# Kernel optimization log

Hardware: AMD Instinct MI355X
Metric: run time of the kernel (lower is better)

## Reference

```python
import jax, jax.numpy as jnp
import numpy as np
from functools import partial

B, H, W = 2, 480, 480
C, HALF = 32, 16
L, WN, PAD = 4, 20, 20

def gelu(x):
    return jax.nn.gelu(x, approximate=False)

def setup_inputs() -> dict:
    key = jax.random.key(0)
    ks = jax.random.split(key, 24)
    scale = 1.0 / (C * C)
    d = {}
    d["input_data"] = jax.random.normal(ks[0], (B, H, W, 1), jnp.float32)
    d["src_data"] = jax.random.normal(ks[1], (B, H, W, 3), jnp.float32)
    # input lifting MLP: sizes [5, 16, 32]
    d["in_w1"] = jax.random.normal(ks[2], (5, HALF), jnp.float32) * 0.1
    d["in_b1"] = jnp.zeros((HALF,), jnp.float32)
    d["in_w2"] = jax.random.normal(ks[3], (HALF, C), jnp.float32) * 0.1
    d["in_b2"] = jnp.zeros((C,), jnp.float32)
    # eps lifting MLP: sizes [3, 16, 32]
    d["eps_w1"] = jax.random.normal(ks[4], (3, HALF), jnp.float32) * 0.1
    d["eps_b1"] = jnp.zeros((HALF,), jnp.float32)
    d["eps_w2"] = jax.random.normal(ks[5], (HALF, C), jnp.float32) * 0.1
    d["eps_b2"] = jnp.zeros((C,), jnp.float32)
    # Fourier layer params, stacked over L layers
    d["fw1"] = jax.random.uniform(ks[6], (L, C, C, WN, WN, 2), jnp.float32) * scale
    d["fw2"] = jax.random.uniform(ks[7], (L, C, C, WN, WN, 2), jnp.float32) * scale
    d["conv_w"] = jax.random.normal(ks[8], (L, C, C), jnp.float32) * 0.05
    d["conv_b"] = jnp.zeros((L, C), jnp.float32)
    # projection MLP: sizes [32, 16, 2]
    d["proj_w1"] = jax.random.normal(ks[9], (C, HALF), jnp.float32) * 0.1
    d["proj_b1"] = jnp.zeros((HALF,), jnp.float32)
    d["proj_w2"] = jax.random.normal(ks[10], (HALF, 2), jnp.float32) * 0.1
    d["proj_b2"] = jnp.zeros((2,), jnp.float32)
    # mask conv 3x3, 1->1 channel
    d["mask_w"] = jax.random.normal(ks[11], (1, 1, 3, 3), jnp.float32) * 0.1
    d["mask_b"] = jnp.zeros((1,), jnp.float32)
    return d

def _grid(b, h, w):
    gx = jnp.broadcast_to(jnp.linspace(0.0, 1.0, h, dtype=jnp.float32)[None, :, None, None], (b, h, w, 1))
    gy = jnp.broadcast_to(jnp.linspace(0.0, 1.0, w, dtype=jnp.float32)[None, None, :, None], (b, h, w, 1))
    return jnp.concatenate([gx, gy], axis=-1)

def _mlp(x, w1, b1, w2, b2):
    # FCLayer(gelu) then FCLayer(linear)
    return gelu(x @ w1 + b1) @ w2 + b2

def _fourier_conv(x, x_eps, w1, w2):
    # x, x_eps: [B, C, Hp, Wp]
    hp, wp = x.shape[-2], x.shape[-1]
    xf = jnp.fft.rfft2(x * x_eps)                       # [B,C,Hp,Wp//2+1] complex
    xr = jnp.stack([xf.real, xf.imag], axis=-1)         # [B,C,Hp,Wp//2+1,2]
    lo = jnp.einsum('bixyz,ioxyz->boxyz', xr[:, :, :WN, :WN, :], w1)
    hi = jnp.einsum('bixyz,ioxyz->boxyz', xr[:, :, -WN:, :WN, :], w2)
    out = jnp.zeros((x.shape[0], w1.shape[1], hp, wp // 2 + 1, 2), jnp.float32)
    out = out.at[:, :, :WN, :WN, :].set(lo)
    out = out.at[:, :, -WN:, :WN, :].set(hi)
    return jnp.fft.irfft2(out[..., 0] + 1j * out[..., 1], s=(hp, wp))

def _forward(input_data, src_data, in_w1, in_b1, in_w2, in_b2,
             eps_w1, eps_b1, eps_w2, eps_b2, fw1, fw2, conv_w, conv_b,
             proj_w1, proj_b1, proj_w2, proj_b2, mask_w, mask_b):
    b, h, w = input_data.shape[0], input_data.shape[1], input_data.shape[2]
    grid = _grid(b, h, w)
    x_in = jnp.concatenate([src_data, grid], axis=-1)       # [B,H,W,5]
    x_eps = jnp.concatenate([input_data, grid], axis=-1)    # [B,H,W,3]
    field = src_data[..., 1:]                               # [B,H,W,2]

    a = _mlp(x_in, in_w1, in_b1, in_w2, in_b2)              # [B,H,W,C]
    a = jnp.transpose(a, (0, 3, 1, 2))                      # [B,C,H,W]
    a = jnp.pad(a, ((0, 0), (0, 0), (0, PAD), (0, PAD)))    # [B,C,H+P,W+P]
    e = _mlp(x_eps, eps_w1, eps_b1, eps_w2, eps_b2)
    e = jnp.transpose(e, (0, 3, 1, 2))
    e = jnp.pad(e, ((0, 0), (0, 0), (0, PAD), (0, PAD)))

    for l in range(L):
        x1 = _fourier_conv(a, e, fw1[l], fw2[l])
        x2 = jnp.einsum('bihw,oi->bohw', a, conv_w[l]) + conv_b[l][None, :, None, None]
        a = x1 + x2
        if l < L - 1:
            a = gelu(a)

    pred = a[..., :-PAD, :-PAD]                             # [B,C,H,W]
    pred = jnp.transpose(pred, (0, 2, 3, 1))                # [B,H,W,C]
    pred = _mlp(pred, proj_w1, proj_b1, proj_w2, proj_b2)   # [B,H,W,2]

    xm = jnp.transpose(input_data, (0, 3, 1, 2))            # [B,1,H,W]
    mask = jax.lax.conv_general_dilated(xm, mask_w, (1, 1), 'SAME',
                                        dimension_numbers=('NCHW', 'OIHW', 'NCHW'))
    mask = mask + mask_b[None, :, None, None]
    mask = jnp.transpose(mask, (0, 2, 3, 1))                # [B,H,W,1] -> broadcasts over 2
    return field * mask + pred

def reference(input_data, src_data, in_w1, in_b1, in_w2, in_b2,
              eps_w1, eps_b1, eps_w2, eps_b2, fw1, fw2, conv_w, conv_b,
              proj_w1, proj_b1, proj_w2, proj_b2, mask_w, mask_b):
    return _forward(input_data, src_data, in_w1, in_b1, in_w2, in_b2,
                    eps_w1, eps_b1, eps_w2, eps_b2, fw1, fw2, conv_w, conv_b,
                    proj_w1, proj_b1, proj_w2, proj_b2, mask_w, mask_b)
```

## Files before the change

### kernel.cpp

```cpp
#include <hip/hip_runtime.h>
#include <hip/hip_bf16.h>

#define BD 2
#define HD 480
#define WD 480
#define CD 32
#define HALFD 16
#define WND 20
#define NP 500
#define PLANE (HD*WD)
#define TWO_PI_OVER_NP 0.012566370614359172954f

typedef __attribute__((ext_vector_type(8))) short bf16x8;
typedef __attribute__((ext_vector_type(4))) float f32x4;

__device__ __forceinline__ float gelu_f(float x) {
    return 0.5f * x * (1.0f + erff(x * 0.70710678118654752f));
}
__device__ __forceinline__ float bfbits2f(short s) {
    unsigned u = ((unsigned)(unsigned short)s) << 16;
    return __uint_as_float(u);
}
__device__ __forceinline__ short bf16s(float v) {
    __hip_bfloat16 b = __float2bfloat16(v);
    return *reinterpret_cast<short*>(&b);
}
__device__ __forceinline__ unsigned pk2(float a, float b) {
    return (unsigned)(unsigned short)bf16s(a) | ((unsigned)(unsigned short)bf16s(b) << 16);
}

__global__ void __launch_bounds__(256) k_ae(
    const float* src, const float* inp,
    const float* iw1, const float* ib1,
    const float* iw2, const float* ib2,
    const float* ew1, const float* eb1,
    const float* ew2, const float* eb2,
    __hip_bfloat16* A, __hip_bfloat16* E)
{
    __shared__ float s_iw1[80], s_ib1[16];
    __shared__ float s_ew1[48], s_eb1[16];
    __shared__ __align__(16) __hip_bfloat16 s_hidA[256 * 24];
    __shared__ __align__(16) __hip_bfloat16 s_hidE[256 * 24];
    __shared__ __align__(16) __hip_bfloat16 s_out[32 * 264];

    int tid = threadIdx.x;
    int lane = tid & 63, wv = tid >> 6;

    if (tid < 80) s_iw1[tid] = iw1[tid];
    if (tid >= 96 && tid < 112) s_ib1[tid - 96] = ib1[tid - 96];
    if (tid >= 128 && tid < 176) s_ew1[tid - 128] = ew1[tid - 128];
    if (tid >= 192 && tid < 208) s_eb1[tid - 192] = eb1[tid - 192];

    int c0 = lane & 15, kg = lane >> 4;
    bf16x8 bIn[2], bEps[2];
    float biasIn[2], biasEps[2];
    #pragma unroll
    for (int nt = 0; nt < 2; nt++) {
        int c = nt * 16 + c0;
        #pragma unroll
        for (int j = 0; j < 8; j++) {
            int k = kg * 8 + j;
            bIn[nt][j]  = (k < 16) ? bf16s(iw2[k * 32 + c]) : (short)0;
            bEps[nt][j] = (k < 16) ? bf16s(ew2[k * 32 + c]) : (short)0;
        }
        biasIn[nt]  = ib2[c];
        biasEps[nt] = eb2[c];
    }
    __syncthreads();

    int gid = blockIdx.x * 256 + tid;
    int b = gid / PLANE;
    int r = gid % PLANE;
    int h = r / WD, w = r % WD;
    float gx = (float)h * (1.0f / 479.0f);
    float gy = (float)w * (1.0f / 479.0f);
    float s0 = src[(size_t)gid * 3 + 0];
    float s1 = src[(size_t)gid * 3 + 1];
    float s2 = src[(size_t)gid * 3 + 2];
    float xi = inp[gid];

    {
        unsigned pk[8];
        #pragma unroll
        for (int j = 0; j < 16; j += 2) {
            float v0 = s_ib1[j]     + s0 * s_iw1[j]     + s1 * s_iw1[16 + j]
                     + s2 * s_iw1[32 + j]     + gx * s_iw1[48 + j]     + gy * s_iw1[64 + j];
            float v1 = s_ib1[j + 1] + s0 * s_iw1[j + 1] + s1 * s_iw1[16 + j + 1]
                     + s2 * s_iw1[32 + j + 1] + gx * s_iw1[48 + j + 1] + gy * s_iw1[64 + j + 1];
            pk[j >> 1] = pk2(gelu_f(v0), gelu_f(v1));
        }
        uint4* d = reinterpret_cast<uint4*>(&s_hidA[tid * 24]);
        d[0] = make_uint4(pk[0], pk[1], pk[2], pk[3]);
        d[1] = make_uint4(pk[4], pk[5], pk[6], pk[7]);
        #pragma unroll
        for (int j = 0; j < 16; j += 2) {
            float v0 = s_eb1[j]     + xi * s_ew1[j]     + gx * s_ew1[16 + j]     + gy * s_ew1[32 + j];
            float v1 = s_eb1[j + 1] + xi * s_ew1[j + 1] + gx * s_ew1[16 + j + 1] + gy * s_ew1[32 + j + 1];
            pk[j >> 1] = pk2(gelu_f(v0), gelu_f(v1));
        }
        uint4* d2 = reinterpret_cast<uint4*>(&s_hidE[tid * 24]);
        d2[0] = make_uint4(pk[0], pk[1], pk[2], pk[3]);
        d2[1] = make_uint4(pk[4], pk[5], pk[6], pk[7]);
    }
    __syncthreads();

    int r0 = (blockIdx.x % 900) * 256;

    #pragma unroll
    for (int pass = 0; pass < 2; pass++) {
        const __hip_bfloat16* hid = pass ? s_hidE : s_hidA;
        #pragma unroll
        for (int t = 0; t < 4; t++) {
            int tile = wv * 4 + t;
            bf16x8 av = {0, 0, 0, 0, 0, 0, 0, 0};
            if (kg < 2)
                av = *reinterpret_cast<const bf16x8*>(&hid[(tile * 16 + c0) * 24 + kg * 8]);
            #pragma unroll
            for (int nt = 0; nt < 2; nt++) {
                f32x4 acc = {0.f, 0.f, 0.f, 0.f};
                bf16x8 bv = pass ? bEps[nt] : bIn[nt];
                acc = __builtin_amdgcn_mfma_f32_16x16x32_bf16(av, bv, acc, 0, 0, 0);
                float bias = pass ? biasEps[nt] : biasIn[nt];
                int ch = nt * 16 + c0;
                int px = tile * 16 + kg * 4;
                unsigned w0 = pk2(acc[0] + bias, acc[1] + bias);
                unsigned w1 = pk2(acc[2] + bias, acc[3] + bias);
                *reinterpret_cast<uint2*>(&s_out[ch * 264 + px]) = make_uint2(w0, w1);
            }
        }
        __syncthreads();
        __hip_bfloat16* dst = (pass ? E : A) + (size_t)b * CD * PLANE + r0;
        #pragma unroll
        for (int i = 0; i < 4; i++) {
            int idx = tid + i * 256;
            int ch = idx >> 5, chunk = idx & 31;
            uint4 v = *reinterpret_cast<const uint4*>(&s_out[ch * 264 + chunk * 8]);
            *reinterpret_cast<uint4*>(&dst[(size_t)ch * PLANE + chunk * 8]) = v;
        }
        __syncthreads();
    }
}

__global__ void k_tables(__hip_bfloat16* T) {
    int e = blockIdx.x * 256 + threadIdx.x;
    if (e >= 435 * 512) return;
    int tile = e >> 9, r = e & 511;
    int lane = r >> 3, j = r & 7;
    float v = 0.0f;
    if (tile < 45) {
        int kt = tile / 3, nt = tile % 3;
        int k = kt * 32 + ((lane >> 4) << 3) + j;
        int n = nt * 16 + (lane & 15);
        if (n < 40) {
            int ky = n >> 1;
            int idx = (k * ky) % NP;
            float ang = (float)idx * TWO_PI_OVER_NP;
            v = (n & 1) ? -sinf(ang) : cosf(ang);
        }
    } else if (tile < 105) {
        int t2 = tile - 45;
        int nt = t2 >> 1, kt = t2 & 1;
        int kk = kt * 32 + ((lane >> 4) << 3) + j;
        int w = nt * 16 + (lane & 15);
        if (kk < 40) {
            int ky = kk >> 1;
            int idx = (ky * w) % NP;
            float ang = (float)idx * TWO_PI_OVER_NP;
            v = (kk & 1) ? -sinf(ang) : cosf(ang);
        }
    } else if (tile < 255) {
        int t2 = tile - 105;
        int kt = t2 / 5, nt = t2 % 5;
        int k = kt * 32 + ((lane >> 4) << 3) + j;
        int n = nt * 16 + (lane & 15);
        int hh = k >> 1, ri = k & 1;
        int kxi = n >> 1, part = n & 1;
        int kx = (kxi < 20) ? kxi : kxi + 460;
        int idx = (kx * hh) % NP;
        float ang = (float)idx * TWO_PI_OVER_NP;
        float c = cosf(ang), s = sinf(ang);
        v = (part == 0) ? (ri == 0 ? c : s) : (ri == 0 ? -s : c);
    } else {
        int t2 = tile - 255;
        int nt = t2 / 3, kt = t2 % 3;
        int k = kt * 32 + ((lane >> 4) << 3) + j;
        int n = nt * 16 + (lane & 15);
        if (k < 80) {
            int kxi = k >> 1, ri = k & 1;
            int hh = n >> 1, part = n & 1;
            int kx = (kxi < 20) ? kxi : kxi + 460;
            int idx = (kx * hh) % NP;
            float ang = (float)idx * TWO_PI_OVER_NP;
            float c = cosf(ang), s = sinf(ang);
            v = (part == 0) ? (ri == 0 ? c : -s) : (ri == 0 ? s : c);
        }
    }
    T[e] = __float2bfloat16(v);
}

__global__ void __launch_bounds__(256) k_F1m(
    const __hip_bfloat16* A, const __hip_bfloat16* E,
    const __hip_bfloat16* Twig, __hip_bfloat16* Y1)
{
    int wv = threadIdx.x >> 6, lane = threadIdx.x & 63;
    int task = blockIdx.x * 4 + wv;
    int bh = task / 6, rem = task % 6;
    int mt = rem & 1, nt = rem >> 1;
    int b = bh / HD, h = bh % HD;
    int c = mt * 16 + (lane & 15);
    int koff = (lane >> 4) << 3;
    size_t base = ((size_t)(b * 32 + c)) * PLANE + (size_t)h * WD + koff;
    const __hip_bfloat16* arow = A + base;
    const __hip_bfloat16* erow = E + base;
    f32x4 acc = {0.f, 0.f, 0.f, 0.f};
    #pragma unroll
    for (int kt = 0; kt < 15; kt++) {
        bf16x8 av = *reinterpret_cast<const bf16x8*>(arow + kt * 32);
        bf16x8 ev = *reinterpret_cast<const bf16x8*>(erow + kt * 32);
        bf16x8 gv;
        #pragma unroll
        for (int j = 0; j < 8; j++)
            gv[j] = bf16s(bfbits2f(av[j]) * bfbits2f(ev[j]));
        bf16x8 bv = *reinterpret_cast<const bf16x8*>(Twig + (((kt * 3 + nt) << 9) + lane * 8));
        acc = __builtin_amdgcn_mfma_f32_16x16x32_bf16(gv, bv, acc, 0, 0, 0);
    }
    int n = nt * 16 + (lane & 15);
    if (n < 40) {
        int ky = n >> 1, part = n & 1;
        int crow = mt * 16 + ((lane >> 4) << 2);
        #pragma unroll
        for (int r = 0; r < 4; r++) {
            int cc = crow + r;
            Y1[((((size_t)(b * 32 + cc)) * WND + ky) * HD + h) * 2 + part] =
                __float2bfloat16(acc[r]);
        }
    }
}

__global__ void __launch_bounds__(64) k_F2m(
    const __hip_bfloat16* Y1, const __hip_bfloat16* Tf2, float* Y2)
{
    int lane = threadIdx.x;
    int task = blockIdx.x;
    int mt = task / 5, nt = task % 5;
    int row = mt * 16 + (lane & 15);
    int koff = (lane >> 4) << 3;
    const __hip_bfloat16* arow = Y1 + (size_t)row * 960 + koff;
    f32x4 acc = {0.f, 0.f, 0.f, 0.f};
    #pragma unroll
    for (int kt = 0; kt < 30; kt++) {
        bf16x8 av = *reinterpret_cast<const bf16x8*>(arow + kt * 32);
        bf16x8 bv = *reinterpret_cast<const bf16x8*>(Tf2 + (((kt * 5 + nt) << 9) + lane * 8));
        acc = __builtin_amdgcn_mfma_f32_16x16x32_bf16(av, bv, acc, 0, 0, 0);
    }
    int n = nt * 16 + (lane & 15);
    int mb = mt * 16 + ((lane >> 4) << 2);
    #pragma unroll
    for (int r = 0; r < 4; r++)
        Y2[(size_t)(mb + r) * 80 + n] = acc[r];
}

__global__ void __launch_bounds__(256) k_mix(
    const float* Y2, __hip_bfloat16* Zb,
    const float* fw1, const float* fw2, int l)
{
    int gid = blockIdx.x * 256 + threadIdx.x;
    int col = gid % 96;
    int row = gid / 96;
    if (col >= 80) { Zb[gid] = __float2bfloat16(0.0f); return; }
    int ky = row % 20;
    int oc = (row / 20) % 32;
    int b = row / 640;
    int z = col & 1;
    int kxi = col >> 1;
    const float* wp;
    int x;
    if (kxi < 20) { wp = fw1; x = kxi; } else { wp = fw2; x = kxi - 20; }
    size_t wbase = ((((size_t)(l * 32) * 32 + oc) * 20 + x) * 20 + ky) * 2 + z;
    const float* y2 = Y2 + ((size_t)b * 32 * 20 + ky) * 80 + kxi * 2 + z;
    float acc = 0.f;
    for (int i = 0; i < 32; i++) {
        float yv = y2[(size_t)i * 1600];
        float wv = wp[wbase + (size_t)i * 25600];
        acc += yv * wv;
    }
    Zb[gid] = __float2bfloat16(acc);
}

__global__ void __launch_bounds__(256) k_I1m(
    const __hip_bfloat16* Zb, const __hip_bfloat16* Ti1, __hip_bfloat16* U)
{
    int wv = threadIdx.x >> 6, lane = threadIdx.x & 63;
    int task = blockIdx.x * 4 + wv;
    int mt = task / 60, nt = task % 60;
    int row = mt * 16 + (lane & 15);
    int koff = (lane >> 4) << 3;
    const __hip_bfloat16* arow = Zb + (size_t)row * 96 + koff;
    f32x4 acc = {0.f, 0.f, 0.f, 0.f};
    #pragma unroll
    for (int kt = 0; kt < 3; kt++) {
        bf16x8 av = *reinterpret_cast<const bf16x8*>(arow + kt * 32);
        bf16x8 bv = *reinterpret_cast<const bf16x8*>(Ti1 + (((nt * 3 + kt) << 9) + lane * 8));
        acc = __builtin_amdgcn_mfma_f32_16x16x32_bf16(av, bv, acc, 0, 0, 0);
    }
    int n = nt * 16 + (lane & 15);
    int mb = mt * 16 + ((lane >> 4) << 2);
    #pragma unroll
    for (int r = 0; r < 4; r++)
        U[(size_t)(mb + r) * 960 + n] = __float2bfloat16(acc[r]);
}

__global__ void __launch_bounds__(512) k_I2F1(
    const __hip_bfloat16* U, __hip_bfloat16* A,
    const __hip_bfloat16* E,
    const float* convw, const float* convb,
    const __hip_bfloat16* TinvF, const __hip_bfloat16* Twig,
    __hip_bfloat16* Y1, int l)
{
    __shared__ __align__(16) __hip_bfloat16 sUf[4 * 512];
    __shared__ __align__(16) __hip_bfloat16 sWf[2 * 512];
    __shared__ __align__(16) __hip_bfloat16 sA[32 * 488];
    __shared__ float sB[CD];
    int tid = threadIdx.x;
    int b = blockIdx.x / HD;
    int h = blockIdx.x % HD;
    if (tid < CD) sB[tid] = convb[l * CD + tid];
    for (int t = tid; t < 2048; t += 512) {
        int j = t & 7, lane = (t >> 3) & 63, ktmt = t >> 9;
        int mt = ktmt >> 1, kt = ktmt & 1;
        int oc = mt * 16 + (lane & 15);
        int kk = kt * 32 + ((lane >> 4) << 3) + j;
        float v = 0.f;
        if (kk < 40) {
            int ky = kk >> 1;
            __hip_bfloat162 u = reinterpret_cast<const __hip_bfloat162*>(U)
                [(((size_t)b * CD + oc) * WND + ky) * HD + h];
            float sc = (ky == 0 ? 1.0f : 2.0f) * (1.0f / 250000.0f);
            v = ((kk & 1) ? __bfloat162float(u.y) : __bfloat162float(u.x)) * sc;
        }
        sUf[t] = __float2bfloat16(v);
    }
    for (int t = tid; t < 1024; t += 512) {
        int j = t & 7, lane = (t >> 3) & 63, mt = t >> 9;
        int oc = mt * 16 + (lane & 15);
        int ic = ((lane >> 4) << 3) + j;
        sWf[t] = __float2bfloat16(convw[(size_t)l * CD * CD + oc * CD + ic]);
    }
    __syncthreads();
    int wv = tid >> 6, lane = tid & 63;
    int c0 = lane & 15, kg = lane >> 4;
    const unsigned short* Ap = reinterpret_cast<const unsigned short*>(A)
        + (size_t)b * CD * PLANE + (size_t)h * WD;
    for (int t = wv; t < 60; t += 8) {
        int mt = t & 1, nt = t >> 1;
        f32x4 acc = {0.f, 0.f, 0.f, 0.f};
        #pragma unroll
        for (int kt = 0; kt < 2; kt++) {
            bf16x8 av = *reinterpret_cast<const bf16x8*>(&sUf[((mt * 2 + kt) << 9) + lane * 8]);
            bf16x8 bv = *reinterpret_cast<const bf16x8*>(TinvF + (((nt * 2 + kt) << 9) + lane * 8));
            acc = __builtin_amdgcn_mfma_f32_16x16x32_bf16(av, bv, acc, 0, 0, 0);
        }
        bf16x8 av2 = *reinterpret_cast<const bf16x8*>(&sWf[(mt << 9) + lane * 8]);
        bf16x8 bv2;
        #pragma unroll
        for (int j = 0; j < 8; j++)
            bv2[j] = (short)Ap[(size_t)(kg * 8 + j) * PLANE + nt * 16 + c0];
        acc = __builtin_amdgcn_mfma_f32_16x16x32_bf16(av2, bv2, acc, 0, 0, 0);
        int w = nt * 16 + c0;
        int ocb = mt * 16 + (kg << 2);
        #pragma unroll
        for (int r = 0; r < 4; r++) {
            short sv = bf16s(gelu_f(acc[r] + sB[ocb + r]));
            sA[(ocb + r) * 488 + w] = *reinterpret_cast<__hip_bfloat16*>(&sv);
        }
    }
    __syncthreads();
    if (wv < 6) {
        int mt = wv & 1, nt = wv >> 1;
        int c = mt * 16 + c0;
        const __hip_bfloat16* erow =
            E + ((size_t)(b * 32 + c)) * PLANE + (size_t)h * WD + (kg << 3);
        const __hip_bfloat16* albase = &sA[c * 488 + (kg << 3)];
        f32x4 acc = {0.f, 0.f, 0.f, 0.f};
        #pragma unroll
        for (int kt = 0; kt < 15; kt++) {
            bf16x8 av = *reinterpret_cast<const bf16x8*>(albase + kt * 32);
            bf16x8 ev = *reinterpret_cast<const bf16x8*>(erow + kt * 32);
            bf16x8 gv;
            #pragma unroll
            for (int j = 0; j < 8; j++)
                gv[j] = bf16s(bfbits2f(av[j]) * bfbits2f(ev[j]));
            bf16x8 bv = *reinterpret_cast<const bf16x8*>(Twig + (((kt * 3 + nt) << 9) + lane * 8));
            acc = __builtin_amdgcn_mfma_f32_16x16x32_bf16(gv, bv, acc, 0, 0, 0);
        }
        int n = nt * 16 + c0;
        if (n < 40) {
            int ky = n >> 1, part = n & 1;
            int crow = mt * 16 + (kg << 2);
            #pragma unroll
            for (int r = 0; r < 4; r++) {
                int cc = crow + r;
                Y1[((((size_t)(b * 32 + cc)) * WND + ky) * HD + h) * 2 + part] =
                    __float2bfloat16(acc[r]);
            }
        }
    } else {
        __hip_bfloat16* Adst = A + (size_t)b * CD * PLANE + (size_t)h * WD;
        for (int t = tid - 384; t < 32 * 60; t += 128) {
            int row = t / 60, chunk = t % 60;
            uint4 v = *reinterpret_cast<const uint4*>(&sA[row * 488 + chunk * 8]);
            *reinterpret_cast<uint4*>(&Adst[(size_t)row * PLANE + chunk * 8]) = v;
        }
    }
}

__global__ void __launch_bounds__(512) k_I2out(
    const __hip_bfloat16* U, const __hip_bfloat16* A,
    const float* convw, const float* convb,
    const __hip_bfloat16* TinvF,
    const float* inp, const float* src,
    const float* pw1, const float* pb1,
    const float* pw2, const float* pb2,
    const float* mw, const float* mb,
    float* out, int l)
{
    __shared__ __align__(16) __hip_bfloat16 sUf[4 * 512];
    __shared__ __align__(16) __hip_bfloat16 sWf[2 * 512];
    __shared__ __align__(16) __hip_bfloat16 sAT[WD * 40];
    __shared__ float sP[WD * 2];
    __shared__ float sB[CD];
    __shared__ float sB1[HALFD], sW2[HALFD * 2], sB2[2], sM[9], sMB[1];
    int tid = threadIdx.x;
    int lane = tid & 63, wv = tid >> 6;
    int c0 = lane & 15, kg = lane >> 4;
    int b = blockIdx.x / HD;
    int h = blockIdx.x % HD;
    if (tid < CD) sB[tid] = convb[l * CD + tid];
    if (tid >= 32 && tid < 48) sB1[tid - 32] = pb1[tid - 32];
    if (tid >= 64 && tid < 96) sW2[tid - 64] = pw2[tid - 64];
    if (tid >= 96 && tid < 98) sB2[tid - 96] = pb2[tid - 96];
    if (tid >= 128 && tid < 137) sM[tid - 128] = mw[tid - 128];
    if (tid == 160) sMB[0] = mb[0];
    bf16x8 bW1;
    #pragma unroll
    for (int j = 0; j < 8; j++)
        bW1[j] = bf16s(pw1[(kg * 8 + j) * 16 + c0]);
    for (int t = tid; t < 2048; t += 512) {
        int j = t & 7, lane2 = (t >> 3) & 63, ktmt = t >> 9;
        int mt = ktmt >> 1, kt = ktmt & 1;
        int oc = mt * 16 + (lane2 & 15);
        int kk = kt * 32 + ((lane2 >> 4) << 3) + j;
        float v = 0.f;
        if (kk < 40) {
            int ky = kk >> 1;
            __hip_bfloat162 u = reinterpret_cast<const __hip_bfloat162*>(U)
                [(((size_t)b * CD + oc) * WND + ky) * HD + h];
            float sc = (ky == 0 ? 1.0f : 2.0f) * (1.0f / 250000.0f);
            v = ((kk & 1) ? __bfloat162float(u.y) : __bfloat162float(u.x)) * sc;
        }
        sUf[t] = __float2bfloat16(v);
    }
    for (int t = tid; t < 1024; t += 512) {
        int j = t & 7, lane2 = (t >> 3) & 63, mt = t >> 9;
        int oc = mt * 16 + (lane2 & 15);
        int ic = ((lane2 >> 4) << 3) + j;
        sWf[t] = __float2bfloat16(convw[(size_t)l * CD * CD + oc * CD + ic]);
    }
    __syncthreads();
    const unsigned short* Ap = reinterpret_cast<const unsigned short*>(A)
        + (size_t)b * CD * PLANE + (size_t)h * WD;
    for (int t = wv; t < 60; t += 8) {
        int mt = t & 1, nt = t >> 1;
        f32x4 acc = {0.f, 0.f, 0.f, 0.f};
        #pragma unroll
        for (int kt = 0; kt < 2; kt++) {
            bf16x8 av = *reinterpret_cast<const bf16x8*>(&sUf[((mt * 2 + kt) << 9) + lane * 8]);
            bf16x8 bv = *reinterpret_cast<const bf16x8*>(TinvF + (((nt * 2 + kt) << 9) + lane * 8));
            acc = __builtin_amdgcn_mfma_f32_16x16x32_bf16(av, bv, acc, 0, 0, 0);
        }
        bf16x8 av2 = *reinterpret_cast<const bf16x8*>(&sWf[(mt << 9) + lane * 8]);
        bf16x8 bv2;
        #pragma unroll
        for (int j = 0; j < 8; j++)
            bv2[j] = (short)Ap[(size_t)(kg * 8 + j) * PLANE + nt * 16 + c0];
        acc = __builtin_amdgcn_mfma_f32_16x16x32_bf16(av2, bv2, acc, 0, 0, 0);
        int w = nt * 16 + c0;
        int ocb = mt * 16 + (kg << 2);
        unsigned q0 = pk2(acc[0] + sB[ocb + 0], acc[1] + sB[ocb + 1]);
        unsigned q1 = pk2(acc[2] + sB[ocb + 2], acc[3] + sB[ocb + 3]);
        *reinterpret_cast<uint2*>(&sAT[w * 40 + ocb]) = make_uint2(q0, q1);
    }
    __syncthreads();
    for (int t = wv; t < 30; t += 8) {
        bf16x8 av = *reinterpret_cast<const bf16x8*>(&sAT[(t * 16 + c0) * 40 + kg * 8]);
        f32x4 acc = {0.f, 0.f, 0.f, 0.f};
        acc = __builtin_amdgcn_mfma_f32_16x16x32_bf16(av, bW1, acc, 0, 0, 0);
        #pragma unroll
        for (int r = 0; r < 4; r++) {
            float hid = gelu_f(acc[r] + sB1[c0]);
            float p0 = hid * sW2[c0 * 2 + 0];
            float p1 = hid * sW2[c0 * 2 + 1];
            #pragma unroll
            for (int m = 1; m < 16; m <<= 1) {
                p0 += __shfl_xor(p0, m, 64);
                p1 += __shfl_xor(p1, m, 64);
            }
            if (c0 == 0) {
                int px = t * 16 + kg * 4 + r;
                sP[px * 2 + 0] = p0 + sB2[0];
                sP[px * 2 + 1] = p1 + sB2[1];
            }
        }
    }
    __syncthreads();
    for (int w = tid; w < WD; w += 512) {
        float p0 = sP[w * 2 + 0];
        float p1 = sP[w * 2 + 1];
        float m = sMB[0];
        #pragma unroll
        for (int dh = 0; dh < 3; dh++) {
            int hh = h + dh - 1;
            #pragma unroll
            for (int dw = 0; dw < 3; dw++) {
                int ww = w + dw - 1;
                if (hh >= 0 && hh < HD && ww >= 0 && ww < WD)
                    m += inp[(size_t)b * PLANE + (size_t)hh * WD + ww] * sM[dh * 3 + dw];
            }
        }
        size_t gid = (size_t)b * PLANE + (size_t)h * WD + w;
        float f0 = src[gid * 3 + 1];
        float f1 = src[gid * 3 + 2];
        out[gid * 2 + 0] = f0 * m + p0;
        out[gid * 2 + 1] = f1 * m + p1;
    }
}

extern "C" void kernel_launch(void* const* d_in, const int* in_sizes, int n_in,
                              void* d_out, int out_size, void* d_ws, size_t ws_size,
                              hipStream_t stream) {
    const float* inp = (const float*)d_in[0];
    const float* src = (const float*)d_in[1];
    const float* iw1 = (const float*)d_in[2];
    const float* ib1 = (const float*)d_in[3];
    const float* iw2 = (const float*)d_in[4];
    const float* ib2 = (const float*)d_in[5];
    const float* ew1 = (const float*)d_in[6];
    const float* eb1 = (const float*)d_in[7];
    const float* ew2 = (const float*)d_in[8];
    const float* eb2 = (const float*)d_in[9];
    const float* fw1 = (const float*)d_in[10];
    const float* fw2 = (const float*)d_in[11];
    const float* cw  = (const float*)d_in[12];
    const float* cb  = (const float*)d_in[13];
    const float* pw1 = (const float*)d_in[14];
    const float* pb1 = (const float*)d_in[15];
    const float* pw2 = (const float*)d_in[16];
    const float* pb2 = (const float*)d_in[17];
    const float* mw  = (const float*)d_in[18];
    const float* mb  = (const float*)d_in[19];

    const size_t NA = (size_t)BD * CD * PLANE;
    __hip_bfloat16* A   = (__hip_bfloat16*)d_ws;
    __hip_bfloat16* E   = A + NA;
    __hip_bfloat16* Y1U = E + NA;
    float* Y2 = (float*)(Y1U + (size_t)BD * CD * WND * HD * 2);
    __hip_bfloat16* Zb = (__hip_bfloat16*)(Y2 + 1280 * 80);
    __hip_bfloat16* Tbl   = Zb + 1280 * 96;
    __hip_bfloat16* Twig  = Tbl;
    __hip_bfloat16* TinvF = Twig + 45 * 512;
    __hip_bfloat16* Tf2   = TinvF + 60 * 512;
    __hip_bfloat16* Ti1   = Tf2 + 150 * 512;

    k_tables<<<870, 256, 0, stream>>>(Tbl);
    k_ae<<<1800, 256, 0, stream>>>(src, inp, iw1, ib1, iw2, ib2,
                                   ew1, eb1, ew2, eb2, A, E);

    k_F1m<<<1440, 256, 0, stream>>>(A, E, Twig, Y1U);
    for (int l = 0; l < 4; l++) {
        k_F2m<<<400, 64, 0, stream>>>(Y1U, Tf2, Y2);
        k_mix<<<480, 256, 0, stream>>>(Y2, Zb, fw1, fw2, l);
        k_I1m<<<1200, 256, 0, stream>>>(Zb, Ti1, Y1U);
        if (l < 3)
            k_I2F1<<<BD * HD, 512, 0, stream>>>(Y1U, A, E, cw, cb, TinvF, Twig,
                                                Y1U, l);
        else
            k_I2out<<<BD * HD, 512, 0, stream>>>(Y1U, A, cw, cb, TinvF,
                                                 inp, src, pw1, pb1, pw2, pb2,
                                                 mw, mb, (float*)d_out, l);
    }
}
```

Measured before the change: 373.4 us.

## Fuse lifting MLPs with first forward DFT stage per image row

Merges the lifting kernel and the first W-direction DFT kernel into one kernel with one block per (batch, row) of 512 threads. The product A*E is formed in shared memory and fed straight into the MFMA DFT, so k_F1m no longer re-reads A and E from global memory and one launch goes away. The cost is fewer, larger blocks (960) holding more shared memory, which lowers occupancy. Only 6 of 8 waves do the DFT stage.

```diff
diff --git a/kernel.cpp b/kernel.cpp
--- a/kernel.cpp
+++ b/kernel.cpp
@@ -29,29 +29,31 @@
     return (unsigned)(unsigned short)bf16s(a) | ((unsigned)(unsigned short)bf16s(b) << 16);
 }
 
-__global__ void __launch_bounds__(256) k_ae(
+__global__ void __launch_bounds__(512) k_aeF1(
     const float* src, const float* inp,
     const float* iw1, const float* ib1,
     const float* iw2, const float* ib2,
     const float* ew1, const float* eb1,
     const float* ew2, const float* eb2,
-    __hip_bfloat16* A, __hip_bfloat16* E)
+    const __hip_bfloat16* Twig,
+    __hip_bfloat16* A, __hip_bfloat16* E, __hip_bfloat16* Y1)
 {
     __shared__ float s_iw1[80], s_ib1[16];
     __shared__ float s_ew1[48], s_eb1[16];
-    __shared__ __align__(16) __hip_bfloat16 s_hidA[256 * 24];
-    __shared__ __align__(16) __hip_bfloat16 s_hidE[256 * 24];
-    __shared__ __align__(16) __hip_bfloat16 s_out[32 * 264];
+    __shared__ __align__(16) __hip_bfloat16 s_hid[480 * 24];
+    __shared__ __align__(16) __hip_bfloat16 sA[32 * 488];
 
     int tid = threadIdx.x;
     int lane = tid & 63, wv = tid >> 6;
+    int c0 = lane & 15, kg = lane >> 4;
+    int b = blockIdx.x / HD;
+    int h = blockIdx.x % HD;
 
     if (tid < 80) s_iw1[tid] = iw1[tid];
     if (tid >= 96 && tid < 112) s_ib1[tid - 96] = ib1[tid - 96];
     if (tid >= 128 && tid < 176) s_ew1[tid - 128] = ew1[tid - 128];
     if (tid >= 192 && tid < 208) s_eb1[tid - 192] = eb1[tid - 192];
 
-    int c0 = lane & 15, kg = lane >> 4;
     bf16x8 bIn[2], bEps[2];
     float biasIn[2], biasEps[2];
     #pragma unroll
@@ -66,20 +68,20 @@
         biasIn[nt]  = ib2[c];
         biasEps[nt] = eb2[c];
     }
-    __syncthreads();
-
-    int gid = blockIdx.x * 256 + tid;
-    int b = gid / PLANE;
-    int r = gid % PLANE;
-    int h = r / WD, w = r % WD;
+
+    float s0 = 0.f, s1 = 0.f, s2 = 0.f, xi = 0.f;
     float gx = (float)h * (1.0f / 479.0f);
-    float gy = (float)w * (1.0f / 479.0f);
-    float s0 = src[(size_t)gid * 3 + 0];
-    float s1 = src[(size_t)gid * 3 + 1];
-    float s2 = src[(size_t)gid * 3 + 2];
-    float xi = inp[gid];
-
-    {
+    float gy = (float)tid * (1.0f / 479.0f);
+    size_t pbase = (size_t)b * PLANE + (size_t)h * WD;
+    if (tid < WD) {
+        s0 = src[(pbase + tid) * 3 + 0];
+        s1 = src[(pbase + tid) * 3 + 1];
+        s2 = src[(pbase + tid) * 3 + 2];
+        xi = inp[pbase + tid];
+    }
+    __syncthreads();
+
+    if (tid < WD) {
         unsigned pk[8];
         #pragma unroll
         for (int j = 0; j < 16; j += 2) {
@@ -89,55 +91,96 @@
                      + s2 * s_iw1[32 + j + 1] + gx * s_iw1[48 + j + 1] + gy * s_iw1[64 + j + 1];
             pk[j >> 1] = pk2(gelu_f(v0), gelu_f(v1));
         }
-        uint4* d = reinterpret_cast<uint4*>(&s_hidA[tid * 24]);
+        uint4* d = reinterpret_cast<uint4*>(&s_hid[tid * 24]);
         d[0] = make_uint4(pk[0], pk[1], pk[2], pk[3]);
         d[1] = make_uint4(pk[4], pk[5], pk[6], pk[7]);
+    }
+    __syncthreads();
+
+    for (int t = wv; t < 60; t += 8) {
+        int tile = t >> 1, nt = t & 1;
+        bf16x8 av = {0, 0, 0, 0, 0, 0, 0, 0};
+        if (kg < 2)
+            av = *reinterpret_cast<const bf16x8*>(&s_hid[(tile * 16 + c0) * 24 + kg * 8]);
+        f32x4 acc = {0.f, 0.f, 0.f, 0.f};
+        acc = __builtin_amdgcn_mfma_f32_16x16x32_bf16(av, bIn[nt], acc, 0, 0, 0);
+        float bias = biasIn[nt];
+        int ch = nt * 16 + c0;
+        int px = tile * 16 + kg * 4;
+        unsigned w0 = pk2(acc[0] + bias, acc[1] + bias);
+        unsigned w1 = pk2(acc[2] + bias, acc[3] + bias);
+        *reinterpret_cast<uint2*>(&sA[ch * 488 + px]) = make_uint2(w0, w1);
+    }
+    __syncthreads();
+
+    {
+        __hip_bfloat16* Adst = A + (size_t)b * CD * PLANE + (size_t)h * WD;
+        for (int t = tid; t < 32 * 60; t += 512) {
+            int row = t / 60, chunk = t % 60;
+            uint4 v = *reinterpret_cast<const uint4*>(&sA[row * 488 + chunk * 8]);
+            *reinterpret_cast<uint4*>(&Adst[(size_t)row * PLANE + chunk * 8]) = v;
+        }
+    }
+    if (tid < WD) {
+        unsigned pk[8];
         #pragma unroll
         for (int j = 0; j < 16; j += 2) {
             float v0 = s_eb1[j]     + xi * s_ew1[j]     + gx * s_ew1[16 + j]     + gy * s_ew1[32 + j];
             float v1 = s_eb1[j + 1] + xi * s_ew1[j + 1] + gx * s_ew1[16 + j + 1] + gy * s_ew1[32 + j + 1];
             pk[j >> 1] = pk2(gelu_f(v0), gelu_f(v1));
         }
-        uint4* d2 = reinterpret_cast<uint4*>(&s_hidE[tid * 24]);
-        d2[0] = make_uint4(pk[0], pk[1], pk[2], pk[3]);
-        d2[1] = make_uint4(pk[4], pk[5], pk[6], pk[7]);
-    }
-    __syncthreads();
-
-    int r0 = (blockIdx.x % 900) * 256;
-
-    #pragma unroll
-    for (int pass = 0; pass < 2; pass++) {
-        const __hip_bfloat16* hid = pass ? s_hidE : s_hidA;
-        #pragma unroll
-        for (int t = 0; t < 4; t++) {
-            int tile = wv * 4 + t;
-            bf16x8 av = {0, 0, 0, 0, 0, 0, 0, 0};
-            if (kg < 2)
-                av = *reinterpret_cast<const bf16x8*>(&hid[(tile * 16 + c0) * 24 + kg * 8]);
+        uint4* d = reinterpret_cast<uint4*>(&s_hid[tid * 24]);
+        d[0] = make_uint4(pk[0], pk[1], pk[2], pk[3]);
+        d[1] = make_uint4(pk[4], pk[5], pk[6], pk[7]);
+    }
+    __syncthreads();
+
+    for (int t = wv; t < 60; t += 8) {
+        int tile = t >> 1, nt = t & 1;
+        bf16x8 av = {0, 0, 0, 0, 0, 0, 0, 0};
+        if (kg < 2)
+            av = *reinterpret_cast<const bf16x8*>(&s_hid[(tile * 16 + c0) * 24 + kg * 8]);
+        f32x4 acc = {0.f, 0.f, 0.f, 0.f};
+        acc = __builtin_amdgcn_mfma_f32_16x16x32_bf16(av, bEps[nt], acc, 0, 0, 0);
+        float bias = biasEps[nt];
+        int ch = nt * 16 + c0;
+        int px = tile * 16 + kg * 4;
+        float e0 = acc[0] + bias, e1 = acc[1] + bias;
+        float e2 = acc[2] + bias, e3 = acc[3] + bias;
+        *reinterpret_cast<uint2*>(&E[(size_t)(b * 32 + ch) * PLANE + (size_t)h * WD + px])
+            = make_uint2(pk2(e0, e1), pk2(e2, e3));
+        uint2 a8 = *reinterpret_cast<const uint2*>(&sA[ch * 488 + px]);
+        float a0 = bfbits2f((short)(a8.x & 0xffff));
+        float a1 = bfbits2f((short)(a8.x >> 16));
+        float a2 = bfbits2f((short)(a8.y & 0xffff));
+        float a3 = bfbits2f((short)(a8.y >> 16));
+        *reinterpret_cast<uint2*>(&sA[ch * 488 + px])
+            = make_uint2(pk2(a0 * e0, a1 * e1), pk2(a2 * e2, a3 * e3));
+    }
+    __syncthreads();
+
+    if (wv < 6) {
+        int mt = wv & 1, nt = wv >> 1;
+        int c = mt * 16 + c0;
+        const __hip_bfloat16* gbase = &sA[c * 488 + (kg << 3)];
+        f32x4 acc = {0.f, 0.f, 0.f, 0.f};
+        #pragma unroll
+        for (int kt = 0; kt < 15; kt++) {
+            bf16x8 gv = *reinterpret_cast<const bf16x8*>(gbase + kt * 32);
+            bf16x8 bv = *reinterpret_cast<const bf16x8*>(Twig + (((kt * 3 + nt) << 9) + lane * 8));
+            acc = __builtin_amdgcn_mfma_f32_16x16x32_bf16(gv, bv, acc, 0, 0, 0);
+        }
+        int n = nt * 16 + c0;
+        if (n < 40) {
+            int ky = n >> 1, part = n & 1;
+            int crow = mt * 16 + (kg << 2);
             #pragma unroll
-            for (int nt = 0; nt < 2; nt++) {
-                f32x4 acc = {0.f, 0.f, 0.f, 0.f};
-                bf16x8 bv = pass ? bEps[nt] : bIn[nt];
-                acc = __builtin_amdgcn_mfma_f32_16x16x32_bf16(av, bv, acc, 0, 0, 0);
-                float bias = pass ? biasEps[nt] : biasIn[nt];
-                int ch = nt * 16 + c0;
-                int px = tile * 16 + kg * 4;
-                unsigned w0 = pk2(acc[0] + bias, acc[1] + bias);
-                unsigned w1 = pk2(acc[2] + bias, acc[3] + bias);
-                *reinterpret_cast<uint2*>(&s_out[ch * 264 + px]) = make_uint2(w0, w1);
+            for (int r = 0; r < 4; r++) {
+                int cc = crow + r;
+                Y1[((((size_t)(b * 32 + cc)) * WND + ky) * HD + h) * 2 + part] =
+                    __float2bfloat16(acc[r]);
             }
         }
-        __syncthreads();
-        __hip_bfloat16* dst = (pass ? E : A) + (size_t)b * CD * PLANE + r0;
-        #pragma unroll
-        for (int i = 0; i < 4; i++) {
-            int idx = tid + i * 256;
-            int ch = idx >> 5, chunk = idx & 31;
-            uint4 v = *reinterpret_cast<const uint4*>(&s_out[ch * 264 + chunk * 8]);
-            *reinterpret_cast<uint4*>(&dst[(size_t)ch * PLANE + chunk * 8]) = v;
-        }
-        __syncthreads();
     }
 }
 
@@ -196,45 +239,6 @@
         }
     }
     T[e] = __float2bfloat16(v);
-}
-
-__global__ void __launch_bounds__(256) k_F1m(
-    const __hip_bfloat16* A, const __hip_bfloat16* E,
-    const __hip_bfloat16* Twig, __hip_bfloat16* Y1)
-{
-    int wv = threadIdx.x >> 6, lane = threadIdx.x & 63;
-    int task = blockIdx.x * 4 + wv;
-    int bh = task / 6, rem = task % 6;
-    int mt = rem & 1, nt = rem >> 1;
-    int b = bh / HD, h = bh % HD;
-    int c = mt * 16 + (lane & 15);
-    int koff = (lane >> 4) << 3;
-    size_t base = ((size_t)(b * 32 + c)) * PLANE + (size_t)h * WD + koff;
-    const __hip_bfloat16* arow = A + base;
-    const __hip_bfloat16* erow = E + base;
-    f32x4 acc = {0.f, 0.f, 0.f, 0.f};
-    #pragma unroll
-    for (int kt = 0; kt < 15; kt++) {
-        bf16x8 av = *reinterpret_cast<const bf16x8*>(arow + kt * 32);
-        bf16x8 ev = *reinterpret_cast<const bf16x8*>(erow + kt * 32);
-        bf16x8 gv;
-        #pragma unroll
-        for (int j = 0; j < 8; j++)
-            gv[j] = bf16s(bfbits2f(av[j]) * bfbits2f(ev[j]));
-        bf16x8 bv = *reinterpret_cast<const bf16x8*>(Twig + (((kt * 3 + nt) << 9) + lane * 8));
-        acc = __builtin_amdgcn_mfma_f32_16x16x32_bf16(gv, bv, acc, 0, 0, 0);
-    }
-    int n = nt * 16 + (lane & 15);
-    if (n < 40) {
-        int ky = n >> 1, part = n & 1;
-        int crow = mt * 16 + ((lane >> 4) << 2);
-        #pragma unroll
-        for (int r = 0; r < 4; r++) {
-            int cc = crow + r;
-            Y1[((((size_t)(b * 32 + cc)) * WND + ky) * HD + h) * 2 + part] =
-                __float2bfloat16(acc[r]);
-        }
-    }
 }
 
 __global__ void __launch_bounds__(64) k_F2m(
@@ -572,10 +576,8 @@
     __hip_bfloat16* Ti1   = Tf2 + 150 * 512;
 
     k_tables<<<870, 256, 0, stream>>>(Tbl);
-    k_ae<<<1800, 256, 0, stream>>>(src, inp, iw1, ib1, iw2, ib2,
-                                   ew1, eb1, ew2, eb2, A, E);
-
-    k_F1m<<<1440, 256, 0, stream>>>(A, E, Twig, Y1U);
+    k_aeF1<<<BD * HD, 512, 0, stream>>>(src, inp, iw1, ib1, iw2, ib2,
+                                        ew1, eb1, ew2, eb2, Twig, A, E, Y1U);
     for (int l = 0; l < 4; l++) {
         k_F2m<<<400, 64, 0, stream>>>(Y1U, Tf2, Y2);
         k_mix<<<480, 256, 0, stream>>>(Y2, Zb, fw1, fw2, l);
```

After: 357.9 us. 4.2% less time.
